# Kernel optimization log

Hardware: AMD Instinct MI355X
Metric: run time of the kernel (lower is better)

## Reference

```python
import jax, jax.numpy as jnp
import numpy as np

MULT = 0.0025
EPS = 1e-6  # torch F.pairwise_distance eps added to the difference


def setup_inputs() -> dict:
    key = jax.random.key(0)
    k1, k2, k3, k4 = jax.random.split(key, 4)
    B, K, N = 256, 51, 8192
    y_hat = jax.random.uniform(k1, (B, K), dtype=jnp.float32)
    y = jax.random.uniform(k2, (B, K), dtype=jnp.float32)
    face = jax.random.normal(k3, (N, 3), dtype=jnp.float32)
    bs_tensor = jax.random.normal(k4, (K, N, 3), dtype=jnp.float32)
    return {"y_hat": y_hat, "y": y, "face": face, "bs_tensor": bs_tensor}


def _reconstruct(w, face, bs_tensor):
    # face: [N,3], bs_tensor: [K,N,3], w: [B,K] -> [B,N,3]
    # Contract over blendshape dim directly (avoids the [B,K,N,3] intermediate).
    return face[None] + jnp.einsum('bk,knd->bnd', w, bs_tensor)


def reference(y_hat, y, face, bs_tensor):
    yh_face = _reconstruct(y_hat, face, bs_tensor)  # [B,N,3]
    y_face = _reconstruct(y, face, bs_tensor)       # [B,N,3]
    # transpose(1,2) -> [B,3,N]; pairwise_distance norms over last dim (N)
    diff = jnp.swapaxes(yh_face, 1, 2) - jnp.swapaxes(y_face, 1, 2) + EPS
    dist = jnp.sqrt(jnp.sum(diff * diff, axis=-1))  # [B,3]
    return jnp.sum(dist) * MULT
```

## Files before the change

kernel.cpp:

```cpp
#include <hip/hip_runtime.h>
#include <math.h>

#define NPTS     8192
#define KDIM     51
#define KPAD     64
#define CHUNKS   64
#define CHUNK_N  128
#define MULT     0.0025f

typedef short short8  __attribute__((ext_vector_type(8)));
typedef float float4v __attribute__((ext_vector_type(4)));

__device__ __forceinline__ unsigned short f32_to_bf16(float f) {
    unsigned int u = __float_as_uint(f);
    unsigned int r = u + 0x7FFFu + ((u >> 16) & 1u);
    return (unsigned short)(r >> 16);
}

__global__ __launch_bounds__(256) void pl_gram(
    const float* __restrict__ bs, float* __restrict__ partial) {
  __shared__ unsigned short lds16[KPAD * 136];

  const int bx  = blockIdx.x;
  const int d   = bx / CHUNKS;
  const int n0  = (bx % CHUNKS) * CHUNK_N;
  const int tid = threadIdx.x;

  unsigned int* lds32 = (unsigned int*)lds16;
  for (int u = tid; u < KPAD * (CHUNK_N / 2); u += 256) {
    int np = u & 63;
    int k  = u >> 6;
    float v0 = 0.0f, v1 = 0.0f;
    if (k < KDIM) {
      const float* p = bs + (size_t)k * (NPTS * 3) + (size_t)(n0 + 2 * np) * 3 + d;
      v0 = p[0];
      v1 = p[3];
    }
    lds32[k * 68 + np] = (unsigned int)f32_to_bf16(v0) |
                         ((unsigned int)f32_to_bf16(v1) << 16);
  }
  __syncthreads();

  const int wave  = tid >> 6;
  const int lane  = tid & 63;
  const int m16   = lane & 15;
  const int quad  = lane >> 4;
  const int rbase = (wave >> 1) * 32;
  const int cbase = (wave & 1) * 32;

  float4v acc00 = {0.f, 0.f, 0.f, 0.f}, acc01 = {0.f, 0.f, 0.f, 0.f};
  float4v acc10 = {0.f, 0.f, 0.f, 0.f}, acc11 = {0.f, 0.f, 0.f, 0.f};

#pragma unroll
  for (int p0 = 0; p0 < CHUNK_N; p0 += 32) {
    const int po = p0 + quad * 8;
    short8 a0 = *(const short8*)&lds16[(rbase +      m16) * 136 + po];
    short8 a1 = *(const short8*)&lds16[(rbase + 16 + m16) * 136 + po];
    short8 b0 = *(const short8*)&lds16[(cbase +      m16) * 136 + po];
    short8 b1 = *(const short8*)&lds16[(cbase + 16 + m16) * 136 + po];
    acc00 = __builtin_amdgcn_mfma_f32_16x16x32_bf16(a0, b0, acc00, 0, 0, 0);
    acc01 = __builtin_amdgcn_mfma_f32_16x16x32_bf16(a0, b1, acc01, 0, 0, 0);
    acc10 = __builtin_amdgcn_mfma_f32_16x16x32_bf16(a1, b0, acc10, 0, 0, 0);
    acc11 = __builtin_amdgcn_mfma_f32_16x16x32_bf16(a1, b1, acc11, 0, 0, 0);
  }

  float* pout = partial + (size_t)bx * 4096;
#pragma unroll
  for (int r = 0; r < 4; ++r) {
    int row0 = rbase + quad * 4 + r;
    int col0 = cbase + m16;
    pout[row0 * 64 + col0]             = acc00[r];
    pout[row0 * 64 + (col0 + 16)]      = acc01[r];
    pout[(row0 + 16) * 64 + col0]      = acc10[r];
    pout[(row0 + 16) * 64 + (col0 + 16)] = acc11[r];
  }
}

__global__ __launch_bounds__(256) void pl_reduce_gram(
    const float* __restrict__ partial, float* __restrict__ G,
    float* __restrict__ out) {
  int e = blockIdx.x * 256 + threadIdx.x;
  int d = e >> 12, el = e & 4095;
  float s = 0.0f;
  for (int c = 0; c < CHUNKS; ++c)
    s += partial[(size_t)(d * CHUNKS + c) * 4096 + el];
  G[e] = s;
  if (e == 0) out[0] = 0.0f;
}

__global__ __launch_bounds__(256) void pl_finalize(
    const float* __restrict__ G, const float* __restrict__ yh,
    const float* __restrict__ yv, float* __restrict__ out) {
  __shared__ float Gl[64 * 65];
  __shared__ float wl[16 * 52];
  __shared__ float red2[16];

  const int bx  = blockIdx.x;
  const int d   = bx >> 4;
  const int b0  = (bx & 15) << 4;
  const int tid = threadIdx.x;

  for (int idx = tid; idx < 4096; idx += 256)
    Gl[(idx >> 6) * 65 + (idx & 63)] = G[d * 4096 + idx];
  for (int idx = tid; idx < 16 * KDIM; idx += 256) {
    int bl = idx / KDIM, k = idx - bl * KDIM;
    int gi = (b0 + bl) * KDIM + k;
    wl[bl * 52 + k] = yh[gi] - yv[gi];
  }
  __syncthreads();

  const int bl = tid >> 4;
  const int j  = tid & 15;
  float pq = 0.0f;
  for (int k1 = j; k1 < KDIM; k1 += 16) {
    float t = 0.0f;
    const float* gr = &Gl[k1 * 65];
    const float* wr = &wl[bl * 52];
#pragma unroll
    for (int k2 = 0; k2 < KDIM; ++k2) t = fmaf(gr[k2], wr[k2], t);
    pq = fmaf(wl[bl * 52 + k1], t, pq);
  }
  for (int off = 8; off; off >>= 1) pq += __shfl_down(pq, off, 16);
  if (j == 0) red2[bl] = sqrtf(pq);
  __syncthreads();
  if (tid == 0) {
    float s = 0.0f;
#pragma unroll
    for (int i = 0; i < 16; ++i) s += red2[i];
    atomicAdd(out, s * MULT);
  }
}

extern "C" void kernel_launch(void* const* d_in, const int* in_sizes, int n_in,
                              void* d_out, int out_size, void* d_ws, size_t ws_size,
                              hipStream_t stream) {
  const float* y_hat = (const float*)d_in[0];
  const float* y     = (const float*)d_in[1];
  const float* bs    = (const float*)d_in[3];
  float* out = (float*)d_out;

  float* partial = (float*)d_ws;
  float* G       = partial + (size_t)3 * CHUNKS * 4096;

  pl_gram<<<3 * CHUNKS, 256, 0, stream>>>(bs, partial);
  pl_reduce_gram<<<48, 256, 0, stream>>>(partial, G, out);
  pl_finalize<<<48, 256, 0, stream>>>(G, y_hat, y, out);
}
```

Measured before the change: 22.60 us.

## Fuse gram reduction and finalize into one kernel with grid barrier

Merges the partial-Gram reduction kernel and the finalize kernel into one launch. An atomic counter acts as a grid-wide barrier across the 48 blocks, so each block reduces its slice of G, waits for all blocks, then reads the full G. The gram kernel now also zeroes the output and the counter, and it fetches the two strided values per point with one unaligned 4-float vector load instead of two scalar loads. The goal is to remove one kernel launch and its gap. The spin barrier relies on all 48 blocks being resident at the same time, and the vector load reads past the last needed value, which can go beyond the end of the buffer on the final point.

```diff
diff --git a/kernel.cpp b/kernel.cpp
--- a/kernel.cpp
+++ b/kernel.cpp
@@ -10,6 +10,7 @@
 
 typedef short short8  __attribute__((ext_vector_type(8)));
 typedef float float4v __attribute__((ext_vector_type(4)));
+typedef float float4a __attribute__((ext_vector_type(4), aligned(4)));
 
 __device__ __forceinline__ unsigned short f32_to_bf16(float f) {
     unsigned int u = __float_as_uint(f);
@@ -18,13 +19,16 @@
 }
 
 __global__ __launch_bounds__(256) void pl_gram(
-    const float* __restrict__ bs, float* __restrict__ partial) {
+    const float* __restrict__ bs, float* __restrict__ partial,
+    unsigned int* __restrict__ ctr, float* __restrict__ out) {
   __shared__ unsigned short lds16[KPAD * 136];
 
   const int bx  = blockIdx.x;
   const int d   = bx / CHUNKS;
   const int n0  = (bx % CHUNKS) * CHUNK_N;
   const int tid = threadIdx.x;
+
+  if (bx == 0 && tid == 0) { out[0] = 0.0f; ctr[0] = 0u; }
 
   unsigned int* lds32 = (unsigned int*)lds16;
   for (int u = tid; u < KPAD * (CHUNK_N / 2); u += 256) {
@@ -33,8 +37,9 @@
     float v0 = 0.0f, v1 = 0.0f;
     if (k < KDIM) {
       const float* p = bs + (size_t)k * (NPTS * 3) + (size_t)(n0 + 2 * np) * 3 + d;
-      v0 = p[0];
-      v1 = p[3];
+      float4a f = *(const float4a*)p;
+      v0 = f[0];
+      v1 = f[3];
     }
     lds32[k * 68 + np] = (unsigned int)f32_to_bf16(v0) |
                          ((unsigned int)f32_to_bf16(v1) << 16);
@@ -69,27 +74,16 @@
   for (int r = 0; r < 4; ++r) {
     int row0 = rbase + quad * 4 + r;
     int col0 = cbase + m16;
-    pout[row0 * 64 + col0]             = acc00[r];
-    pout[row0 * 64 + (col0 + 16)]      = acc01[r];
-    pout[(row0 + 16) * 64 + col0]      = acc10[r];
+    pout[row0 * 64 + col0]               = acc00[r];
+    pout[row0 * 64 + (col0 + 16)]        = acc01[r];
+    pout[(row0 + 16) * 64 + col0]        = acc10[r];
     pout[(row0 + 16) * 64 + (col0 + 16)] = acc11[r];
   }
 }
 
-__global__ __launch_bounds__(256) void pl_reduce_gram(
+__global__ __launch_bounds__(256) void pl_reduce_finalize(
     const float* __restrict__ partial, float* __restrict__ G,
-    float* __restrict__ out) {
-  int e = blockIdx.x * 256 + threadIdx.x;
-  int d = e >> 12, el = e & 4095;
-  float s = 0.0f;
-  for (int c = 0; c < CHUNKS; ++c)
-    s += partial[(size_t)(d * CHUNKS + c) * 4096 + el];
-  G[e] = s;
-  if (e == 0) out[0] = 0.0f;
-}
-
-__global__ __launch_bounds__(256) void pl_finalize(
-    const float* __restrict__ G, const float* __restrict__ yh,
+    unsigned int* __restrict__ ctr, const float* __restrict__ yh,
     const float* __restrict__ yv, float* __restrict__ out) {
   __shared__ float Gl[64 * 65];
   __shared__ float wl[16 * 52];
@@ -100,13 +94,31 @@
   const int b0  = (bx & 15) << 4;
   const int tid = threadIdx.x;
 
-  for (int idx = tid; idx < 4096; idx += 256)
-    Gl[(idx >> 6) * 65 + (idx & 63)] = G[d * 4096 + idx];
+  {
+    const int e_d = ((bx & 15) << 8) + tid;
+    const float* p = partial + (size_t)(d * CHUNKS) * 4096 + e_d;
+    float s = 0.0f;
+    for (int c = 0; c < CHUNKS; ++c) s += p[(size_t)c * 4096];
+    G[d * 4096 + e_d] = s;
+  }
+
   for (int idx = tid; idx < 16 * KDIM; idx += 256) {
     int bl = idx / KDIM, k = idx - bl * KDIM;
     int gi = (b0 + bl) * KDIM + k;
     wl[bl * 52 + k] = yh[gi] - yv[gi];
   }
+  __syncthreads();
+  if (tid == 0) {
+    __threadfence();
+    __hip_atomic_fetch_add(ctr, 1u, __ATOMIC_ACQ_REL, __HIP_MEMORY_SCOPE_AGENT);
+    while (__hip_atomic_load(ctr, __ATOMIC_ACQUIRE, __HIP_MEMORY_SCOPE_AGENT) < 48u)
+      __builtin_amdgcn_s_sleep(2);
+  }
+  __syncthreads();
+  __threadfence();
+
+  for (int idx = tid; idx < 4096; idx += 256)
+    Gl[(idx >> 6) * 65 + (idx & 63)] = G[d * 4096 + idx];
   __syncthreads();
 
   const int bl = tid >> 4;
@@ -139,10 +151,10 @@
   const float* bs    = (const float*)d_in[3];
   float* out = (float*)d_out;
 
-  float* partial = (float*)d_ws;
-  float* G       = partial + (size_t)3 * CHUNKS * 4096;
+  float* partial    = (float*)d_ws;
+  float* G          = partial + (size_t)3 * CHUNKS * 4096;
+  unsigned int* ctr = (unsigned int*)(G + 3 * 4096);
 
-  pl_gram<<<3 * CHUNKS, 256, 0, stream>>>(bs, partial);
-  pl_reduce_gram<<<48, 256, 0, stream>>>(partial, G, out);
-  pl_finalize<<<48, 256, 0, stream>>>(G, y_hat, y, out);
+  pl_gram<<<3 * CHUNKS, 256, 0, stream>>>(bs, partial, ctr, out);
+  pl_reduce_finalize<<<48, 256, 0, stream>>>(partial, G, ctr, y_hat, y, out);
 }
```

Result: slower. 26.47 us (+17.1%).
